# Kernel optimization log

Measured on AMD Instinct MI355X. Metric: run time of the kernel, lower is better.

Reference implementation:

```python
import jax, jax.numpy as jnp
import numpy as np

F_TOT = 108
OUT_CH = 5
GNN_IN = 5


def setup_inputs() -> dict:
    key = jax.random.key(0)
    ks = jax.random.split(key, 24)
    B, S, N, E = 16, 1, 20000, 320000
    s = 0.1  # param init scale
    d = {}
    d["x"] = jax.random.normal(ks[0], (B, S, N, F_TOT), jnp.float32)
    d["edge_index"] = jax.random.randint(ks[1], (2, E), 0, N, dtype=jnp.int32)
    # four Conv1d(1, 5, k=24) branches
    for i, nm in enumerate(["t", "r", "tp", "ssr"]):
        d[f"w_{nm}"] = s * jax.random.normal(ks[2 + 2 * i], (OUT_CH, 1, 24), jnp.float32)
        d[f"b_{nm}"] = s * jax.random.normal(ks[3 + 2 * i], (OUT_CH,), jnp.float32)
    # fc1: 32 -> 20, fc2: 20 -> 5
    d["fc1_w"] = s * jax.random.normal(ks[10], (20, 12 + 4 * OUT_CH), jnp.float32)
    d["fc1_b"] = s * jax.random.normal(ks[11], (20,), jnp.float32)
    d["fc2_w"] = s * jax.random.normal(ks[12], (GNN_IN, 20), jnp.float32)
    d["fc2_b"] = s * jax.random.normal(ks[13], (GNN_IN,), jnp.float32)
    # SAGEConv(5 -> 20): lin_l (with bias, applied to mean-aggregated neighbors), lin_r (no bias, root)
    d["g1_wl"] = s * jax.random.normal(ks[14], (20, GNN_IN), jnp.float32)
    d["g1_bl"] = s * jax.random.normal(ks[15], (20,), jnp.float32)
    d["g1_wr"] = s * jax.random.normal(ks[16], (20, GNN_IN), jnp.float32)
    # SAGEConv(20 -> 1)
    d["g2_wl"] = s * jax.random.normal(ks[17], (1, 20), jnp.float32)
    d["g2_bl"] = s * jax.random.normal(ks[18], (1,), jnp.float32)
    d["g2_wr"] = s * jax.random.normal(ks[19], (1, 20), jnp.float32)
    return d


def _branch(xs, w, b):
    # Conv1d(in=1, out=5, k=24) over a length-24 window == a single dot product per channel.
    # xs: [NB, 24], w: [5, 1, 24] -> [NB, 5], then ReLU
    return jax.nn.relu(jnp.einsum('nk,ok->no', xs, w[:, 0, :]) + b)


def _sage(h, src, dst, wl, bl, wr, n_nodes):
    # PyG SAGEConv with mean aggregation: out = lin_l(mean_{j in N(i)} x_j) + lin_r(x_i)
    # h: [B, N, d]
    msg = jnp.transpose(h[:, src, :], (1, 0, 2))                    # [E, B, d]
    agg = jax.ops.segment_sum(msg, dst, num_segments=n_nodes)       # [N, B, d]
    deg = jax.ops.segment_sum(jnp.ones((src.shape[0],), h.dtype), dst, num_segments=n_nodes)
    mean = jnp.transpose(agg, (1, 0, 2)) / jnp.maximum(deg, 1.0)[None, :, None]  # [B, N, d]
    return mean @ wl.T + bl + h @ wr.T


def reference(x, edge_index, w_t, b_t, w_r, b_r, w_tp, b_tp, w_ssr, b_ssr,
              fc1_w, fc1_b, fc2_w, fc2_b, g1_wl, g1_bl, g1_wr, g2_wl, g2_bl, g2_wr):
    B, S, N, F = x.shape
    src, dst = edge_index[0], edge_index[1]
    # permute(2,0,1,3).reshape(N*B, S, F); S == 1
    xs = jnp.transpose(x, (2, 0, 1, 3)).reshape(N * B, S, F)[:, 0, :]  # [NB, 108]
    out_t = _branch(xs[:, 12:36], w_t, b_t)
    out_r = _branch(xs[:, 36:60], w_r, b_r)
    out_tp = _branch(xs[:, 60:84], w_tp, b_tp)
    out_ssr = _branch(xs[:, 84:108], w_ssr, b_ssr)
    feat = jnp.concatenate([xs[:, :12], out_t, out_r, out_tp, out_ssr], axis=1)  # [NB, 32]
    h = jax.nn.relu(feat @ fc1_w.T + fc1_b) @ fc2_w.T + fc2_b                    # [NB, 5]
    h = jnp.transpose(h.reshape(N, B, -1), (1, 0, 2))                            # [B, N, 5]
    h = _sage(h, src, dst, g1_wl, g1_bl, g1_wr, N)                               # [B, N, 20]
    h = _sage(h, src, dst, g2_wl, g2_bl, g2_wr, N)                               # [B, N, 1]
    return jnp.transpose(h, (0, 2, 1))                                           # [B, 1, N]
```

## Files before the change

### kernel.cpp

```cpp
#include <hip/hip_runtime.h>


#define F1W 500
#define F1B 1160
#define CO  1180
#define FEAT 1266
#define HL   3378

__global__ void k_zero(int* __restrict__ cnt, int N) {
  int n = blockIdx.x * blockDim.x + threadIdx.x;
  if (n < N) cnt[n] = 0;
}

__global__ void k_count(const int* __restrict__ dst, int E, int* __restrict__ cnt) {
  int e = blockIdx.x * blockDim.x + threadIdx.x;
  if (e < E) atomicAdd(&cnt[dst[e]], 1);
}

__global__ __launch_bounds__(1024) void k_scan(
    const int* __restrict__ cnt, int N,
    int* __restrict__ row_ptr, int* __restrict__ cursor,
    const float* __restrict__ f2w, const float* __restrict__ f2b,
    const float* __restrict__ g1_wl, const float* __restrict__ g1_bl,
    const float* __restrict__ g1_wr, const float* __restrict__ g2_wl,
    const float* __restrict__ g2_wr, float* __restrict__ coef) {
  int t = threadIdx.x;

  if (t < 21) {
    float a[5], r1[5], c[5], r2[5];
#pragma unroll
    for (int k = 0; k < 5; ++k) { a[k] = 0.f; r1[k] = 0.f; c[k] = 0.f; r2[k] = 0.f; }
#pragma unroll
    for (int j = 0; j < 20; ++j) {
      float wl2 = g2_wl[j], wr2 = g2_wr[j];
#pragma unroll
      for (int k = 0; k < 5; ++k) {
        float wl1 = g1_wl[j * 5 + k], wr1 = g1_wr[j * 5 + k];
        a[k]  = fmaf(wl2, wl1, a[k]);
        r1[k] = fmaf(wr2, wl1, r1[k]);
        c[k]  = fmaf(wl2, wr1, c[k]);
        r2[k] = fmaf(wr2, wr1, r2[k]);
      }
    }
    if (t < 20) {
      float A = 0.f, R1 = 0.f, C = 0.f, R2 = 0.f;
#pragma unroll
      for (int k = 0; k < 5; ++k) {
        float w = f2w[k * 20 + t];
        A  = fmaf(a[k],  w, A);
        R1 = fmaf(r1[k], w, R1);
        C  = fmaf(c[k],  w, C);
        R2 = fmaf(r2[k], w, R2);
      }
      coef[t] = A; coef[20 + t] = R1; coef[40 + t] = C; coef[60 + t] = R2;
    } else {
      float ca = 0.f, cr1 = 0.f, cc = 0.f, cr2 = 0.f;
#pragma unroll
      for (int k = 0; k < 5; ++k) {
        float b = f2b[k];
        ca = fmaf(a[k], b, ca);  cr1 = fmaf(r1[k], b, cr1);
        cc = fmaf(c[k], b, cc);  cr2 = fmaf(r2[k], b, cr2);
      }
      coef[80] = ca; coef[81] = cr1; coef[82] = cc; coef[83] = cr2;
      float kb1 = 0.f, kb2 = 0.f;
#pragma unroll
      for (int j = 0; j < 20; ++j) {
        kb1 = fmaf(g2_wl[j], g1_bl[j], kb1);
        kb2 = fmaf(g2_wr[j], g1_bl[j], kb2);
      }
      coef[84] = kb1; coef[85] = kb2;
    }
  }

  __shared__ int part[1024];
  int chunk = (N + 1023) / 1024;
  int s0 = t * chunk, s1 = min(N, s0 + chunk);
  int sum = 0;
  for (int i = s0; i < s1; ++i) sum += cnt[i];
  part[t] = sum;
  __syncthreads();
  for (int off = 1; off < 1024; off <<= 1) {
    int v = (t >= off) ? part[t - off] : 0;
    __syncthreads();
    part[t] += v;
    __syncthreads();
  }
  int run = (t == 0) ? 0 : part[t - 1];
  for (int i = s0; i < s1; ++i) {
    row_ptr[i] = run; cursor[i] = run;
    run += cnt[i];
  }
  if (s1 == N) row_ptr[N] = run;
}

__global__ void k_scatter(const int* __restrict__ src, const int* __restrict__ dst, int E,
                          int* __restrict__ cursor, int* __restrict__ adj) {
  int e = blockIdx.x * blockDim.x + threadIdx.x;
  if (e < E) {
    int pos = atomicAdd(&cursor[dst[e]], 1);
    adj[pos] = src[e];
  }
}

__global__ __launch_bounds__(256) void k_mlp(
    const float* __restrict__ x,
    const float* __restrict__ w_t, const float* __restrict__ b_t,
    const float* __restrict__ w_r, const float* __restrict__ b_r,
    const float* __restrict__ w_tp, const float* __restrict__ b_tp,
    const float* __restrict__ w_ssr, const float* __restrict__ b_ssr,
    const float* __restrict__ f1w, const float* __restrict__ f1b,
    const float* __restrict__ coef,
    float2* __restrict__ F1v, float2* __restrict__ F2v, int N, int rows) {
  __shared__ float S[4978];
  const int t = threadIdx.x;
  const int q = t & 3, r = t >> 2;
  int rr = blockIdx.x * 64 + r;
  bool live = rr < rows;
  if (!live) rr = rows - 1;

  const float4* xv = reinterpret_cast<const float4*>(x + (size_t)rr * 108);
  float4 bv[6];
#pragma unroll
  for (int i = 0; i < 6; ++i) bv[i] = xv[3 + 6 * q + i];
  float4 pv = make_float4(0.f, 0.f, 0.f, 0.f);
  if (q > 0) pv = xv[q - 1];

  if (t < 120) {
    S[t] = w_t[t]; S[120 + t] = w_r[t]; S[240 + t] = w_tp[t]; S[360 + t] = w_ssr[t];
  }
  if (t < 5) {
    S[480 + t] = b_t[t]; S[485 + t] = b_r[t];
    S[490 + t] = b_tp[t]; S[495 + t] = b_ssr[t];
  }
  for (int i = t; i < 640; i += 256) {
    int o = i >> 5, k = i & 31;
    S[F1W + o * 33 + k] = f1w[i];
  }
  if (t < 20) S[F1B + t] = f1b[t];
  if (t >= 128 && t < 128 + 86) S[CO + t - 128] = coef[t - 128];
  __syncthreads();

  float acc[5];
#pragma unroll
  for (int o = 0; o < 5; ++o) acc[o] = S[480 + q * 5 + o];
#pragma unroll
  for (int i = 0; i < 6; ++i) {
    float4 w4 = bv[i];
#pragma unroll
    for (int o = 0; o < 5; ++o) {
      const int wb = q * 120 + o * 24 + 4 * i;
      acc[o] = fmaf(w4.x, S[wb + 0], acc[o]);
      acc[o] = fmaf(w4.y, S[wb + 1], acc[o]);
      acc[o] = fmaf(w4.z, S[wb + 2], acc[o]);
      acc[o] = fmaf(w4.w, S[wb + 3], acc[o]);
    }
  }
  float* fr = &S[FEAT + r * 33];
  if (q > 0) {
    fr[4 * (q - 1) + 0] = pv.x; fr[4 * (q - 1) + 1] = pv.y;
    fr[4 * (q - 1) + 2] = pv.z; fr[4 * (q - 1) + 3] = pv.w;
  }
#pragma unroll
  for (int o = 0; o < 5; ++o) fr[12 + q * 5 + o] = fmaxf(acc[o], 0.f);
  __syncthreads();

  float a2[5];
#pragma unroll
  for (int j = 0; j < 5; ++j) a2[j] = S[F1B + q * 5 + j];
#pragma unroll
  for (int i = 0; i < 32; ++i) {
    float f = fr[i];
#pragma unroll
    for (int j = 0; j < 5; ++j)
      a2[j] = fmaf(f, S[F1W + (q * 5 + j) * 33 + i], a2[j]);
  }
  float* hr = &S[HL + r * 25];
#pragma unroll
  for (int j = 0; j < 5; ++j) hr[q * 5 + j] = fmaxf(a2[j], 0.f);
  __syncthreads();

  float s = S[CO + 80 + q];
#pragma unroll
  for (int i = 0; i < 20; ++i) s = fmaf(hr[i], S[CO + q * 20 + i], s);
  hr[20 + q] = s;
  __syncthreads();

  if (q == 0 && live) {
    int b = rr / N;
    int n = rr - b * N;
    F1v[n * 16 + b] = make_float2(hr[20], hr[21]);
    F2v[n * 16 + b] = make_float2(hr[22], hr[23]);
  }
}

__global__ void k_agg1(const int* __restrict__ row_ptr, const int* __restrict__ adj,
                       const float2* __restrict__ F1v, const float2* __restrict__ F2v,
                       float* __restrict__ W, float* __restrict__ V, int N) {
  int t = blockIdx.x * blockDim.x + threadIdx.x;
  int g = t >> 4, b = t & 15;
  if (g >= N) return;
  int beg = row_ptr[g], end = row_ptr[g + 1];
  float sa = 0.f, sb = 0.f;
  for (int c = beg; c < end; c += 16) {
    int idx = c + b;
    int a = adj[idx < end ? idx : end - 1];
    int m = min(16, end - c);
    for (int k = 0; k < m; ++k) {
      int s = __shfl(a, k, 16);
      float2 f = F1v[s * 16 + b];
      sa += f.x; sb += f.y;
    }
  }
  float inv = 1.0f / fmaxf((float)(end - beg), 1.0f);
  float2 f2 = F2v[t];
  W[t] = sa * inv + f2.x;
  V[t] = sb * inv;
}

__global__ __launch_bounds__(256) void k_agg2(
    const int* __restrict__ row_ptr, const int* __restrict__ adj,
    const float* __restrict__ W, const float* __restrict__ V,
    const float2* __restrict__ F2v, const float* __restrict__ coef,
    const float* __restrict__ g2_bl, float* __restrict__ out, int N) {
  __shared__ float tile[16][17];
  int t = blockIdx.x * 256 + threadIdx.x;
  int g = t >> 4, b = t & 15;
  float r = 0.f;
  if (g < N) {
    int beg = row_ptr[g], end = row_ptr[g + 1];
    float sw = 0.f;
    for (int c = beg; c < end; c += 16) {
      int idx = c + b;
      int a = adj[idx < end ? idx : end - 1];
      int m = min(16, end - c);
      for (int k = 0; k < m; ++k) {
        int s = __shfl(a, k, 16);
        sw += W[s * 16 + b];
      }
    }
    int deg = end - beg;
    float inv = 1.0f / fmaxf((float)deg, 1.0f);
    float chi = deg > 0 ? 1.f : 0.f;
    r = sw * inv + V[t] + F2v[t].y + coef[84] * chi + coef[85] + g2_bl[0];
  }
  int gl = (threadIdx.x >> 4);
  tile[b][gl] = r;
  __syncthreads();
  int b2 = threadIdx.x >> 4;
  int gl2 = threadIdx.x & 15;
  int n2 = blockIdx.x * 16 + gl2;
  if (n2 < N) out[(size_t)b2 * N + n2] = tile[b2][gl2];
}

extern "C" void kernel_launch(void* const* d_in, const int* in_sizes, int n_in,
                              void* d_out, int out_size, void* d_ws, size_t ws_size,
                              hipStream_t stream) {
  const float* x     = (const float*)d_in[0];
  const int*   ei    = (const int*)d_in[1];
  const float* w_t   = (const float*)d_in[2];
  const float* b_t   = (const float*)d_in[3];
  const float* w_r   = (const float*)d_in[4];
  const float* b_r   = (const float*)d_in[5];
  const float* w_tp  = (const float*)d_in[6];
  const float* b_tp  = (const float*)d_in[7];
  const float* w_ssr = (const float*)d_in[8];
  const float* b_ssr = (const float*)d_in[9];
  const float* f1w   = (const float*)d_in[10];
  const float* f1b   = (const float*)d_in[11];
  const float* f2w   = (const float*)d_in[12];
  const float* f2b   = (const float*)d_in[13];
  const float* g1_wl = (const float*)d_in[14];
  const float* g1_bl = (const float*)d_in[15];
  const float* g1_wr = (const float*)d_in[16];
  const float* g2_wl = (const float*)d_in[17];
  const float* g2_bl = (const float*)d_in[18];
  const float* g2_wr = (const float*)d_in[19];
  float* out = (float*)d_out;

  const int E = in_sizes[1] / 2;
  const int N = out_size / 16;
  const int rows = out_size;
  const int* src = ei;
  const int* dst = ei + E;

  float* ws  = (float*)d_ws;
  float2* F1v = (float2*)ws;
  float2* F2v = F1v + (size_t)16 * N;
  float*  W   = (float*)(F2v + (size_t)16 * N);
  float*  V   = W + (size_t)16 * N;
  float*  coef = V + (size_t)16 * N;
  int* cnt     = (int*)(coef + 128);
  int* row_ptr = cnt + N;
  int* cursor  = row_ptr + N + 1;
  int* adj     = cursor + N;

  int nb16 = (N * 16 + 255) / 256;

  k_zero<<<(N + 255) / 256, 256, 0, stream>>>(cnt, N);
  k_count<<<(E + 255) / 256, 256, 0, stream>>>(dst, E, cnt);
  k_scan<<<1, 1024, 0, stream>>>(cnt, N, row_ptr, cursor,
                                 f2w, f2b, g1_wl, g1_bl, g1_wr, g2_wl, g2_wr, coef);
  k_scatter<<<(E + 255) / 256, 256, 0, stream>>>(src, dst, E, cursor, adj);
  k_mlp<<<(rows + 63) / 64, 256, 0, stream>>>(
      x, w_t, b_t, w_r, b_r, w_tp, b_tp, w_ssr, b_ssr,
      f1w, f1b, coef, F1v, F2v, N, rows);
  k_agg1<<<nb16, 256, 0, stream>>>(row_ptr, adj, F1v, F2v, W, V, N);
  k_agg2<<<nb16, 256, 0, stream>>>(row_ptr, adj, W, V, F2v, coef, g2_bl, out, N);
}
```

Before: 145.5 us.

## Coalesce x loads via LDS staging, fuse fc layers with shuffles, unroll gathers

The MLP kernel now loads each block's 64 rows of x as one contiguous run of float4s, stages them in padded LDS and reads them back per thread, instead of each thread fetching its own strided slices. The fc1/coef stage keeps hidden values in registers and reduces partial dot products across the 4-thread group with shuffles, which removes two shared-memory round trips and two barriers. The neighbor-gather loops in both aggregation kernels are unrolled by 4 so more independent loads are in flight. The grid now uses rows/64 with no tail guard, which assumes rows is a multiple of 64, and the larger LDS footprint may reduce occupancy.

```diff
diff --git a/kernel.cpp b/kernel.cpp
--- a/kernel.cpp
+++ b/kernel.cpp
@@ -1,11 +1,11 @@
 #include <hip/hip_runtime.h>
 
 
-#define F1W 500
-#define F1B 1160
-#define CO  1180
-#define FEAT 1266
-#define HL   3378
+#define PAD 132
+#define XB  0
+#define CV  8448
+#define WB  9984
+#define LDS_TOT 11250
 
 __global__ void k_zero(int* __restrict__ cnt, int N) {
   int n = blockIdx.x * blockDim.x + threadIdx.x;
@@ -110,86 +110,110 @@
     const float* __restrict__ w_ssr, const float* __restrict__ b_ssr,
     const float* __restrict__ f1w, const float* __restrict__ f1b,
     const float* __restrict__ coef,
-    float2* __restrict__ F1v, float2* __restrict__ F2v, int N, int rows) {
-  __shared__ float S[4978];
+    float2* __restrict__ F1v, float2* __restrict__ F2v, int N) {
+  __shared__ float S[LDS_TOT];
   const int t = threadIdx.x;
   const int q = t & 3, r = t >> 2;
-  int rr = blockIdx.x * 64 + r;
-  bool live = rr < rows;
-  if (!live) rr = rows - 1;
-
-  const float4* xv = reinterpret_cast<const float4*>(x + (size_t)rr * 108);
-  float4 bv[6];
-#pragma unroll
-  for (int i = 0; i < 6; ++i) bv[i] = xv[3 + 6 * q + i];
-  float4 pv = make_float4(0.f, 0.f, 0.f, 0.f);
-  if (q > 0) pv = xv[q - 1];
+  const size_t base = (size_t)blockIdx.x * 64;
+
+  float4 ld[7];
+  const float4* xs = reinterpret_cast<const float4*>(x + base * 108);
+#pragma unroll
+  for (int i = 0; i < 7; ++i) {
+    int c = i * 256 + t;
+    ld[i] = xs[c < 1728 ? c : 1727];
+  }
 
   if (t < 120) {
-    S[t] = w_t[t]; S[120 + t] = w_r[t]; S[240 + t] = w_tp[t]; S[360 + t] = w_ssr[t];
+    S[WB + t] = w_t[t]; S[WB + 120 + t] = w_r[t];
+    S[WB + 240 + t] = w_tp[t]; S[WB + 360 + t] = w_ssr[t];
   }
   if (t < 5) {
-    S[480 + t] = b_t[t]; S[485 + t] = b_r[t];
-    S[490 + t] = b_tp[t]; S[495 + t] = b_ssr[t];
+    S[WB + 480 + t] = b_t[t]; S[WB + 485 + t] = b_r[t];
+    S[WB + 490 + t] = b_tp[t]; S[WB + 495 + t] = b_ssr[t];
   }
   for (int i = t; i < 640; i += 256) {
     int o = i >> 5, k = i & 31;
-    S[F1W + o * 33 + k] = f1w[i];
-  }
-  if (t < 20) S[F1B + t] = f1b[t];
-  if (t >= 128 && t < 128 + 86) S[CO + t - 128] = coef[t - 128];
+    S[WB + 500 + o * 33 + k] = f1w[i];
+  }
+  if (t < 20) S[WB + 1160 + t] = f1b[t];
+  if (t >= 128 && t < 128 + 86) S[WB + 1180 + t - 128] = coef[t - 128];
+
+#pragma unroll
+  for (int i = 0; i < 7; ++i) {
+    int c = i * 256 + t;
+    if (c < 1728) {
+      int row = c / 27, part = c - row * 27;
+      *reinterpret_cast<float4*>(&S[XB + row * PAD + part * 4]) = ld[i];
+    }
+  }
   __syncthreads();
 
+  const float* xr = &S[XB + r * PAD];
   float acc[5];
 #pragma unroll
-  for (int o = 0; o < 5; ++o) acc[o] = S[480 + q * 5 + o];
+  for (int o = 0; o < 5; ++o) acc[o] = S[WB + 480 + q * 5 + o];
 #pragma unroll
   for (int i = 0; i < 6; ++i) {
-    float4 w4 = bv[i];
+    float4 w4 = *reinterpret_cast<const float4*>(xr + 12 + 24 * q + 4 * i);
 #pragma unroll
     for (int o = 0; o < 5; ++o) {
-      const int wb = q * 120 + o * 24 + 4 * i;
-      acc[o] = fmaf(w4.x, S[wb + 0], acc[o]);
-      acc[o] = fmaf(w4.y, S[wb + 1], acc[o]);
-      acc[o] = fmaf(w4.z, S[wb + 2], acc[o]);
-      acc[o] = fmaf(w4.w, S[wb + 3], acc[o]);
-    }
-  }
-  float* fr = &S[FEAT + r * 33];
-  if (q > 0) {
-    fr[4 * (q - 1) + 0] = pv.x; fr[4 * (q - 1) + 1] = pv.y;
-    fr[4 * (q - 1) + 2] = pv.z; fr[4 * (q - 1) + 3] = pv.w;
-  }
-#pragma unroll
-  for (int o = 0; o < 5; ++o) fr[12 + q * 5 + o] = fmaxf(acc[o], 0.f);
+      float4 cw = *reinterpret_cast<const float4*>(&S[WB + q * 120 + o * 24 + 4 * i]);
+      acc[o] = fmaf(w4.x, cw.x, acc[o]);
+      acc[o] = fmaf(w4.y, cw.y, acc[o]);
+      acc[o] = fmaf(w4.z, cw.z, acc[o]);
+      acc[o] = fmaf(w4.w, cw.w, acc[o]);
+    }
+  }
+#pragma unroll
+  for (int o = 0; o < 5; ++o) S[CV + r * 24 + q * 5 + o] = fmaxf(acc[o], 0.f);
   __syncthreads();
 
-  float a2[5];
-#pragma unroll
-  for (int j = 0; j < 5; ++j) a2[j] = S[F1B + q * 5 + j];
-#pragma unroll
-  for (int i = 0; i < 32; ++i) {
-    float f = fr[i];
+  float h[5];
+#pragma unroll
+  for (int j = 0; j < 5; ++j) h[j] = S[WB + 1160 + q * 5 + j];
+#pragma unroll
+  for (int i = 0; i < 12; ++i) {
+    float f = xr[i];
 #pragma unroll
     for (int j = 0; j < 5; ++j)
-      a2[j] = fmaf(f, S[F1W + (q * 5 + j) * 33 + i], a2[j]);
-  }
-  float* hr = &S[HL + r * 25];
-#pragma unroll
-  for (int j = 0; j < 5; ++j) hr[q * 5 + j] = fmaxf(a2[j], 0.f);
-  __syncthreads();
-
-  float s = S[CO + 80 + q];
-#pragma unroll
-  for (int i = 0; i < 20; ++i) s = fmaf(hr[i], S[CO + q * 20 + i], s);
-  hr[20 + q] = s;
-  __syncthreads();
-
-  if (q == 0 && live) {
-    int b = rr / N;
-    int n = rr - b * N;
-    F1v[n * 16 + b] = make_float2(hr[20], hr[21]);
-    F2v[n * 16 + b] = make_float2(hr[22], hr[23]);
+      h[j] = fmaf(f, S[WB + 500 + (q * 5 + j) * 33 + i], h[j]);
+  }
+#pragma unroll
+  for (int i = 12; i < 32; ++i) {
+    float f = S[CV + r * 24 + (i - 12)];
+#pragma unroll
+    for (int j = 0; j < 5; ++j)
+      h[j] = fmaf(f, S[WB + 500 + (q * 5 + j) * 33 + i], h[j]);
+  }
+#pragma unroll
+  for (int j = 0; j < 5; ++j) h[j] = fmaxf(h[j], 0.f);
+
+  float pf[4];
+#pragma unroll
+  for (int f = 0; f < 4; ++f) {
+    float s = 0.f;
+#pragma unroll
+    for (int j = 0; j < 5; ++j)
+      s = fmaf(h[j], S[WB + 1180 + f * 20 + q * 5 + j], s);
+    pf[f] = s;
+  }
+#pragma unroll
+  for (int f = 0; f < 4; ++f) {
+    pf[f] += __shfl_xor(pf[f], 1, 4);
+    pf[f] += __shfl_xor(pf[f], 2, 4);
+  }
+
+  if (q == 0) {
+    size_t rr = base + r;
+    int b = (int)(rr / N);
+    int n = (int)(rr - (size_t)b * N);
+    float s0 = pf[0] + S[WB + 1180 + 80];
+    float s1 = pf[1] + S[WB + 1180 + 81];
+    float s2 = pf[2] + S[WB + 1180 + 82];
+    float s3 = pf[3] + S[WB + 1180 + 83];
+    F1v[n * 16 + b] = make_float2(s0, s1);
+    F2v[n * 16 + b] = make_float2(s2, s3);
   }
 }
 
@@ -205,15 +229,24 @@
     int idx = c + b;
     int a = adj[idx < end ? idx : end - 1];
     int m = min(16, end - c);
-    for (int k = 0; k < m; ++k) {
+    int k = 0;
+    for (; k + 4 <= m; k += 4) {
+      int s0 = __shfl(a, k, 16),     s1 = __shfl(a, k + 1, 16);
+      int s2 = __shfl(a, k + 2, 16), s3 = __shfl(a, k + 3, 16);
+      float2 f0 = F1v[s0 * 16 + b], f1 = F1v[s1 * 16 + b];
+      float2 f2 = F1v[s2 * 16 + b], f3 = F1v[s3 * 16 + b];
+      sa += (f0.x + f1.x) + (f2.x + f3.x);
+      sb += (f0.y + f1.y) + (f2.y + f3.y);
+    }
+    for (; k < m; ++k) {
       int s = __shfl(a, k, 16);
       float2 f = F1v[s * 16 + b];
       sa += f.x; sb += f.y;
     }
   }
   float inv = 1.0f / fmaxf((float)(end - beg), 1.0f);
-  float2 f2 = F2v[t];
-  W[t] = sa * inv + f2.x;
+  float2 f2v = F2v[t];
+  W[t] = sa * inv + f2v.x;
   V[t] = sb * inv;
 }
 
@@ -233,7 +266,13 @@
       int idx = c + b;
       int a = adj[idx < end ? idx : end - 1];
       int m = min(16, end - c);
-      for (int k = 0; k < m; ++k) {
+      int k = 0;
+      for (; k + 4 <= m; k += 4) {
+        int s0 = __shfl(a, k, 16),     s1 = __shfl(a, k + 1, 16);
+        int s2 = __shfl(a, k + 2, 16), s3 = __shfl(a, k + 3, 16);
+        sw += (W[s0 * 16 + b] + W[s1 * 16 + b]) + (W[s2 * 16 + b] + W[s3 * 16 + b]);
+      }
+      for (; k < m; ++k) {
         int s = __shfl(a, k, 16);
         sw += W[s * 16 + b];
       }
@@ -301,9 +340,9 @@
   k_scan<<<1, 1024, 0, stream>>>(cnt, N, row_ptr, cursor,
                                  f2w, f2b, g1_wl, g1_bl, g1_wr, g2_wl, g2_wr, coef);
   k_scatter<<<(E + 255) / 256, 256, 0, stream>>>(src, dst, E, cursor, adj);
-  k_mlp<<<(rows + 63) / 64, 256, 0, stream>>>(
+  k_mlp<<<rows / 64, 256, 0, stream>>>(
       x, w_t, b_t, w_r, b_r, w_tp, b_tp, w_ssr, b_ssr,
-      f1w, f1b, coef, F1v, F2v, N, rows);
+      f1w, f1b, coef, F1v, F2v, N);
   k_agg1<<<nb16, 256, 0, stream>>>(row_ptr, adj, F1v, F2v, W, V, N);
   k_agg2<<<nb16, 256, 0, stream>>>(row_ptr, adj, W, V, F2v, coef, g2_bl, out, N);
 }
```

New measurement: 141.9 us. 1.02x faster.

## Use shuffles for final projection, vectorize LDS loads, unroll gather loops

Applied to the files above, without the earlier changes.

The MLP kernel now finishes the last projection with a 4-lane shuffle reduction instead of an extra LDS round trip and two barriers. It reads conv weights from LDS as float4, drops the bounds guard (assuming rows is a multiple of 64), and adds an occupancy hint to the launch bounds. The aggregation kernels replace the shuffle-broadcast neighbor loop with direct adj loads, unrolled by 16 into two accumulators. The zeroing kernel becomes a memset. Dropping the guard is only correct when rows divides evenly by 64.

```diff
diff --git a/kernel.cpp b/kernel.cpp
--- a/kernel.cpp
+++ b/kernel.cpp
@@ -1,16 +1,8 @@
 #include <hip/hip_runtime.h>
 
 
-#define F1W 500
-#define F1B 1160
-#define CO  1180
-#define FEAT 1266
-#define HL   3378
-
-__global__ void k_zero(int* __restrict__ cnt, int N) {
-  int n = blockIdx.x * blockDim.x + threadIdx.x;
-  if (n < N) cnt[n] = 0;
-}
+#define WFEAT 1266
+#define LDS_TOT 3378
 
 __global__ void k_count(const int* __restrict__ dst, int E, int* __restrict__ cnt) {
   int e = blockIdx.x * blockDim.x + threadIdx.x;
@@ -102,7 +94,7 @@
   }
 }
 
-__global__ __launch_bounds__(256) void k_mlp(
+__global__ __launch_bounds__(256, 6) void k_mlp(
     const float* __restrict__ x,
     const float* __restrict__ w_t, const float* __restrict__ b_t,
     const float* __restrict__ w_r, const float* __restrict__ b_r,
@@ -110,13 +102,11 @@
     const float* __restrict__ w_ssr, const float* __restrict__ b_ssr,
     const float* __restrict__ f1w, const float* __restrict__ f1b,
     const float* __restrict__ coef,
-    float2* __restrict__ F1v, float2* __restrict__ F2v, int N, int rows) {
-  __shared__ float S[4978];
+    float2* __restrict__ F1v, float2* __restrict__ F2v, int N) {
+  __shared__ float S[LDS_TOT + 64 * 33];
   const int t = threadIdx.x;
   const int q = t & 3, r = t >> 2;
-  int rr = blockIdx.x * 64 + r;
-  bool live = rr < rows;
-  if (!live) rr = rows - 1;
+  const int rr = blockIdx.x * 64 + r;
 
   const float4* xv = reinterpret_cast<const float4*>(x + (size_t)rr * 108);
   float4 bv[6];
@@ -126,7 +116,8 @@
   if (q > 0) pv = xv[q - 1];
 
   if (t < 120) {
-    S[t] = w_t[t]; S[120 + t] = w_r[t]; S[240 + t] = w_tp[t]; S[360 + t] = w_ssr[t];
+    S[t] = w_t[t]; S[120 + t] = w_r[t];
+    S[240 + t] = w_tp[t]; S[360 + t] = w_ssr[t];
   }
   if (t < 5) {
     S[480 + t] = b_t[t]; S[485 + t] = b_r[t];
@@ -134,10 +125,10 @@
   }
   for (int i = t; i < 640; i += 256) {
     int o = i >> 5, k = i & 31;
-    S[F1W + o * 33 + k] = f1w[i];
-  }
-  if (t < 20) S[F1B + t] = f1b[t];
-  if (t >= 128 && t < 128 + 86) S[CO + t - 128] = coef[t - 128];
+    S[500 + o * 33 + k] = f1w[i];
+  }
+  if (t < 20) S[1160 + t] = f1b[t];
+  if (t >= 128 && t < 128 + 86) S[1180 + t - 128] = coef[t - 128];
   __syncthreads();
 
   float acc[5];
@@ -148,14 +139,14 @@
     float4 w4 = bv[i];
 #pragma unroll
     for (int o = 0; o < 5; ++o) {
-      const int wb = q * 120 + o * 24 + 4 * i;
-      acc[o] = fmaf(w4.x, S[wb + 0], acc[o]);
-      acc[o] = fmaf(w4.y, S[wb + 1], acc[o]);
-      acc[o] = fmaf(w4.z, S[wb + 2], acc[o]);
-      acc[o] = fmaf(w4.w, S[wb + 3], acc[o]);
-    }
-  }
-  float* fr = &S[FEAT + r * 33];
+      float4 cw = *reinterpret_cast<const float4*>(&S[q * 120 + o * 24 + 4 * i]);
+      acc[o] = fmaf(w4.x, cw.x, acc[o]);
+      acc[o] = fmaf(w4.y, cw.y, acc[o]);
+      acc[o] = fmaf(w4.z, cw.z, acc[o]);
+      acc[o] = fmaf(w4.w, cw.w, acc[o]);
+    }
+  }
+  float* fr = &S[WFEAT + r * 33];
   if (q > 0) {
     fr[4 * (q - 1) + 0] = pv.x; fr[4 * (q - 1) + 1] = pv.y;
     fr[4 * (q - 1) + 2] = pv.z; fr[4 * (q - 1) + 3] = pv.w;
@@ -164,32 +155,39 @@
   for (int o = 0; o < 5; ++o) fr[12 + q * 5 + o] = fmaxf(acc[o], 0.f);
   __syncthreads();
 
-  float a2[5];
-#pragma unroll
-  for (int j = 0; j < 5; ++j) a2[j] = S[F1B + q * 5 + j];
+  float h[5];
+#pragma unroll
+  for (int j = 0; j < 5; ++j) h[j] = S[1160 + q * 5 + j];
 #pragma unroll
   for (int i = 0; i < 32; ++i) {
     float f = fr[i];
 #pragma unroll
     for (int j = 0; j < 5; ++j)
-      a2[j] = fmaf(f, S[F1W + (q * 5 + j) * 33 + i], a2[j]);
-  }
-  float* hr = &S[HL + r * 25];
-#pragma unroll
-  for (int j = 0; j < 5; ++j) hr[q * 5 + j] = fmaxf(a2[j], 0.f);
-  __syncthreads();
-
-  float s = S[CO + 80 + q];
-#pragma unroll
-  for (int i = 0; i < 20; ++i) s = fmaf(hr[i], S[CO + q * 20 + i], s);
-  hr[20 + q] = s;
-  __syncthreads();
-
-  if (q == 0 && live) {
+      h[j] = fmaf(f, S[500 + (q * 5 + j) * 33 + i], h[j]);
+  }
+#pragma unroll
+  for (int j = 0; j < 5; ++j) h[j] = fmaxf(h[j], 0.f);
+
+  float pf[4];
+#pragma unroll
+  for (int f = 0; f < 4; ++f) {
+    float s = 0.f;
+#pragma unroll
+    for (int j = 0; j < 5; ++j)
+      s = fmaf(h[j], S[1180 + f * 20 + q * 5 + j], s);
+    pf[f] = s;
+  }
+#pragma unroll
+  for (int f = 0; f < 4; ++f) {
+    pf[f] += __shfl_xor(pf[f], 1, 4);
+    pf[f] += __shfl_xor(pf[f], 2, 4);
+  }
+
+  if (q == 0) {
     int b = rr / N;
     int n = rr - b * N;
-    F1v[n * 16 + b] = make_float2(hr[20], hr[21]);
-    F2v[n * 16 + b] = make_float2(hr[22], hr[23]);
+    F1v[n * 16 + b] = make_float2(pf[0] + S[1180 + 80], pf[1] + S[1180 + 81]);
+    F2v[n * 16 + b] = make_float2(pf[2] + S[1180 + 82], pf[3] + S[1180 + 83]);
   }
 }
 
@@ -200,20 +198,27 @@
   int g = t >> 4, b = t & 15;
   if (g >= N) return;
   int beg = row_ptr[g], end = row_ptr[g + 1];
-  float sa = 0.f, sb = 0.f;
-  for (int c = beg; c < end; c += 16) {
-    int idx = c + b;
-    int a = adj[idx < end ? idx : end - 1];
-    int m = min(16, end - c);
-    for (int k = 0; k < m; ++k) {
-      int s = __shfl(a, k, 16);
-      float2 f = F1v[s * 16 + b];
-      sa += f.x; sb += f.y;
-    }
-  }
+  float sa = 0.f, sb = 0.f, sa2 = 0.f, sb2 = 0.f;
+  int c = beg;
+  for (; c + 16 <= end; c += 16) {
+#pragma unroll
+    for (int k = 0; k < 16; k += 2) {
+      int s0 = adj[c + k], s1 = adj[c + k + 1];
+      float2 f0 = F1v[s0 * 16 + b];
+      float2 f1 = F1v[s1 * 16 + b];
+      sa += f0.x; sb += f0.y;
+      sa2 += f1.x; sb2 += f1.y;
+    }
+  }
+  for (; c < end; ++c) {
+    int s = adj[c];
+    float2 f = F1v[s * 16 + b];
+    sa += f.x; sb += f.y;
+  }
+  sa += sa2; sb += sb2;
   float inv = 1.0f / fmaxf((float)(end - beg), 1.0f);
-  float2 f2 = F2v[t];
-  W[t] = sa * inv + f2.x;
+  float2 f2v = F2v[t];
+  W[t] = sa * inv + f2v.x;
   V[t] = sb * inv;
 }
 
@@ -228,16 +233,21 @@
   float r = 0.f;
   if (g < N) {
     int beg = row_ptr[g], end = row_ptr[g + 1];
-    float sw = 0.f;
-    for (int c = beg; c < end; c += 16) {
-      int idx = c + b;
-      int a = adj[idx < end ? idx : end - 1];
-      int m = min(16, end - c);
-      for (int k = 0; k < m; ++k) {
-        int s = __shfl(a, k, 16);
-        sw += W[s * 16 + b];
-      }
-    }
+    float sw = 0.f, sw2 = 0.f;
+    int c = beg;
+    for (; c + 16 <= end; c += 16) {
+#pragma unroll
+      for (int k = 0; k < 16; k += 2) {
+        int s0 = adj[c + k], s1 = adj[c + k + 1];
+        sw += W[s0 * 16 + b];
+        sw2 += W[s1 * 16 + b];
+      }
+    }
+    for (; c < end; ++c) {
+      int s = adj[c];
+      sw += W[s * 16 + b];
+    }
+    sw += sw2;
     int deg = end - beg;
     float inv = 1.0f / fmaxf((float)deg, 1.0f);
     float chi = deg > 0 ? 1.f : 0.f;
@@ -296,14 +306,14 @@
 
   int nb16 = (N * 16 + 255) / 256;
 
-  k_zero<<<(N + 255) / 256, 256, 0, stream>>>(cnt, N);
+  hipMemsetAsync(cnt, 0, (size_t)N * sizeof(int), stream);
   k_count<<<(E + 255) / 256, 256, 0, stream>>>(dst, E, cnt);
   k_scan<<<1, 1024, 0, stream>>>(cnt, N, row_ptr, cursor,
                                  f2w, f2b, g1_wl, g1_bl, g1_wr, g2_wl, g2_wr, coef);
   k_scatter<<<(E + 255) / 256, 256, 0, stream>>>(src, dst, E, cursor, adj);
-  k_mlp<<<(rows + 63) / 64, 256, 0, stream>>>(
+  k_mlp<<<rows / 64, 256, 0, stream>>>(
       x, w_t, b_t, w_r, b_r, w_tp, b_tp, w_ssr, b_ssr,
-      f1w, f1b, coef, F1v, F2v, N, rows);
+      f1w, f1b, coef, F1v, F2v, N);
   k_agg1<<<nb16, 256, 0, stream>>>(row_ptr, adj, F1v, F2v, W, V, N);
   k_agg2<<<nb16, 256, 0, stream>>>(row_ptr, adj, W, V, F2v, coef, g2_bl, out, N);
 }
```

New measurement: 285.5 us. +96.2%, slower.
